# Kernel tuning notes

Hardware: AMD Instinct MI355X
Metric: run time of the kernel (lower is better)

Reference implementation:

```python
import jax, jax.numpy as jnp
import numpy as np

N = 500_000          # n_nodes
E = 16_000_000       # n_edges (avg degree 32)
F0 = 3               # INIT_DIM, input feature dim
H = 32               # hidden units
N_MID = 6            # num_layers=8 -> 1 first + 6 mid + 1 last
ALPHA = 0.9          # self.ALHPA in the original


def setup_inputs() -> dict:
    key = jax.random.key(0)
    ks = jax.random.split(key, 10)
    s = 0.1  # glorot-ish scale for tiny dims
    x = jax.random.normal(ks[0], (N, F0), jnp.float32)
    rows = jax.random.randint(ks[1], (E,), 0, N, jnp.int32)
    cols = jax.random.randint(ks[2], (E,), 0, N, jnp.int32)
    # normalized adjacency values (positive, small, like D^-1/2 A D^-1/2)
    vals = jax.random.uniform(ks[3], (E,), jnp.float32) * 0.1
    w_init0 = jax.random.normal(ks[4], (F0, F0), jnp.float32) * s
    w_x0 = jax.random.normal(ks[5], (F0, H), jnp.float32) * s
    w_init_mid = jax.random.normal(ks[6], (N_MID, F0, H), jnp.float32) * s
    w_x_mid = jax.random.normal(ks[7], (N_MID, H, H), jnp.float32) * s
    w_init_last = jax.random.normal(ks[8], (F0, H), jnp.float32) * s
    w_x_last = jax.random.normal(ks[9], (H, 1), jnp.float32) * s
    return dict(x=x, rows=rows, cols=cols, vals=vals,
                w_init0=w_init0, w_x0=w_x0,
                w_init_mid=w_init_mid, w_x_mid=w_x_mid,
                w_init_last=w_init_last, w_x_last=w_x_last)


def _spmm(rows, cols, vals, x):
    # sparse [N,N] @ dense [N,F] via COO gather + segment scatter-add
    return jax.ops.segment_sum(vals[:, None] * x[cols], rows, num_segments=N)


def _layer(h, x0, rows, cols, vals, w_init, w_x, act):
    agg = _spmm(rows, cols, vals, h)                       # [N, F]
    blend = ALPHA * agg + (1.0 - ALPHA) * (x0 @ w_init)    # alpha-blended residual
    return act(blend @ w_x)                                # dense transform + activation


def reference(x, rows, cols, vals, w_init0, w_x0, w_init_mid, w_x_mid,
              w_init_last, w_x_last):
    x0 = x
    h = _layer(x, x0, rows, cols, vals, w_init0, w_x0, jax.nn.relu)
    for i in range(N_MID):  # fixed small loop over structurally distinct layers
        h = _layer(h, x0, rows, cols, vals, w_init_mid[i], w_x_mid[i], jax.nn.relu)
    return _layer(h, x0, rows, cols, vals, w_init_last, w_x_last, jax.nn.sigmoid)
```

## Files before the change

### kernel.cpp

```cpp
#include <hip/hip_runtime.h>
#include <hip/hip_fp16.h>

#define NN 500000
#define NE 16000000
#define HD 32
#define NMID 6
#define F0 3

#define RPB 1024
#define NBUK ((NN + RPB - 1) / RPB)
#define GRID_P 2048
#define EBLK ((NE + GRID_P - 1) / GRID_P)
#define CAP 21504

static constexpr float ALPHA = 0.9f;
static constexpr float OMA = 1.0f - 0.9f;
static constexpr float VENC = 8191.0f / 0.1f;
static constexpr float VDEC = 0.1f / 8191.0f;

static __device__ __forceinline__ float pk_val(unsigned int w) {
    return (float)(w >> 19) * VDEC;
}

__global__ void prep_pack(const float* __restrict__ w_init_mid,
                          const float* __restrict__ w_x_mid,
                          const float* __restrict__ w_init_last,
                          const float* __restrict__ w_x_last,
                          float4* __restrict__ wpk,
                          float2* __restrict__ wc2,
                          float* __restrict__ wcl) {
    int t = blockIdx.x * 512 + threadIdx.x;
    if (t < 5 * 256) {
        int i = t >> 8, r = t & 255, k = r >> 4, f = r & 15;
        const float* W = w_x_mid + (size_t)(i + 1) * HD * HD;
        wpk[t] = make_float4(W[(2 * k) * HD + 2 * f], W[(2 * k) * HD + 2 * f + 1],
                             W[(2 * k + 1) * HD + 2 * f], W[(2 * k + 1) * HD + 2 * f + 1]);
    } else if (t < 5 * 256 + NMID * 48) {
        int r = t - 1280;
        int i = r / 48, rr = r % 48, k = rr >> 4, f = rr & 15;
        const float* wi = w_init_mid + (size_t)i * F0 * HD;
        const float* wx = w_x_mid + (size_t)i * HD * HD;
        float a = 0.f, b = 0.f;
        for (int j = 0; j < HD; ++j) {
            a += wi[k * HD + j] * wx[j * HD + 2 * f];
            b += wi[k * HD + j] * wx[j * HD + 2 * f + 1];
        }
        wc2[r] = make_float2(OMA * a, OMA * b);
    } else if (t < 1280 + NMID * 48 + F0) {
        int k = t - (1280 + NMID * 48);
        float a = 0.f;
        for (int j = 0; j < HD; ++j) a += w_init_last[k * HD + j] * w_x_last[j];
        wcl[k] = OMA * a;
    }
}

__global__ void prep_xh(const float* __restrict__ x, uint2* __restrict__ xh) {
    int n = blockIdx.x * 256 + threadIdx.x;
    if (n >= NN) return;
    __half2 lo = __floats2half2_rn(x[n * 3 + 0], x[n * 3 + 1]);
    __half2 hi = __floats2half2_rn(x[n * 3 + 2], 0.f);
    xh[n] = make_uint2(*reinterpret_cast<unsigned int*>(&lo),
                       *reinterpret_cast<unsigned int*>(&hi));
}

__global__ void bucket_hist(const int* __restrict__ rows, int* __restrict__ cnt) {
    __shared__ int lh[512];
    int tid = threadIdx.x;
    lh[tid] = 0;
    __syncthreads();
    int e0 = blockIdx.x * EBLK;
    int e1 = min(e0 + EBLK, NE);
    for (int e = e0 + tid; e < e1; e += 512)
        atomicAdd(&lh[rows[e] >> 10], 1);
    __syncthreads();
    if (tid < NBUK && lh[tid]) atomicAdd(&cnt[tid], lh[tid]);
}

__global__ void scan_buckets(int* __restrict__ cnt) {
    __shared__ int s[512];
    int tid = threadIdx.x;
    int v = (tid < NBUK) ? cnt[tid] : 0;
    s[tid] = v;
    __syncthreads();
    for (int off = 1; off < 512; off <<= 1) {
        int t = (tid >= off) ? s[tid - off] : 0;
        __syncthreads();
        s[tid] += t;
        __syncthreads();
    }
    if (tid < NBUK) cnt[tid] = s[tid] - v;
}

__global__ void p1_scatter(const int* __restrict__ rows, const int* __restrict__ cols,
                           const float* __restrict__ vals, int* __restrict__ tail,
                           int2* __restrict__ tmp) {
    __shared__ int lh[512], gb[512], lp[512];
    int tid = threadIdx.x;
    lh[tid] = 0;
    __syncthreads();
    int e0 = blockIdx.x * EBLK;
    int e1 = min(e0 + EBLK, NE);
    for (int e = e0 + tid; e < e1; e += 512)
        atomicAdd(&lh[rows[e] >> 10], 1);
    __syncthreads();
    if (tid < NBUK && lh[tid]) gb[tid] = atomicAdd(&tail[tid], lh[tid]);
    lp[tid] = 0;
    __syncthreads();
    for (int e = e0 + tid; e < e1; e += 512) {
        int r = rows[e];
        int b = r >> 10;
        int loc = atomicAdd(&lp[b], 1);
        int pos = gb[b] + loc;
        tmp[pos] = make_int2(((r & (RPB - 1)) << 19) | cols[e], __float_as_int(vals[e]));
    }
}

__global__ void __launch_bounds__(1024) p2_csr(const int* __restrict__ tail,
                                               const int2* __restrict__ tmp,
                                               int* __restrict__ rp,
                                               unsigned int* __restrict__ espk) {
    __shared__ int a[RPB];
    __shared__ int tl[RPB];
    __shared__ unsigned int lbuf[CAP];
    int b = blockIdx.x, tid = threadIdx.x;
    int estart = (b == 0) ? 0 : tail[b - 1];
    int eend = tail[b];
    a[tid] = 0;
    __syncthreads();
    for (int e = estart + tid; e < eend; e += RPB)
        atomicAdd(&a[(unsigned)tmp[e].x >> 19], 1);
    __syncthreads();
    int myc = a[tid];
    for (int off = 1; off < RPB; off <<= 1) {
        int t = (tid >= off) ? a[tid - off] : 0;
        __syncthreads();
        a[tid] += t;
        __syncthreads();
    }
    int rend = estart + a[tid];
    tl[tid] = rend - myc;
    int grow = b * RPB + tid;
    if (grow < NN) rp[grow] = rend;
    __syncthreads();
    int mid = estart + a[511];
    #pragma unroll
    for (int half = 0; half < 2; ++half) {
        int hstart = (half == 0) ? estart : mid;
        int hend   = (half == 0) ? mid : eend;
        int cnt = hend - hstart;
        if (cnt <= CAP) {
            for (int e = estart + tid; e < eend; e += RPB) {
                int2 t = tmp[e];
                int rl = (unsigned)t.x >> 19;
                if ((rl >> 9) == half) {
                    int pos = atomicAdd(&tl[rl], 1);
                    unsigned int q = __float2uint_rn(__int_as_float(t.y) * VENC);
                    lbuf[pos - hstart] = (q << 19) | ((unsigned)t.x & 0x7FFFFu);
                }
            }
            __syncthreads();
            for (int i = tid; i < cnt; i += RPB)
                espk[hstart + i] = lbuf[i];
            __syncthreads();
        } else {
            for (int e = estart + tid; e < eend; e += RPB) {
                int2 t = tmp[e];
                int rl = (unsigned)t.x >> 19;
                if ((rl >> 9) == half) {
                    int pos = atomicAdd(&tl[rl], 1);
                    unsigned int q = __float2uint_rn(__int_as_float(t.y) * VENC);
                    espk[pos] = (q << 19) | ((unsigned)t.x & 0x7FFFFu);
                }
            }
            __syncthreads();
        }
    }
}

__global__ void layer1_fused(const int* __restrict__ rp, const unsigned int* __restrict__ espk,
                             const uint2* __restrict__ xh,
                             const float* __restrict__ x0, const float* __restrict__ w_init0,
                             const float* __restrict__ w_x0, const float* __restrict__ w_x1,
                             unsigned int* __restrict__ gh_out) {
    int tid = blockIdx.x * 256 + threadIdx.x;
    int n = tid >> 5, f = tid & 31;
    if (n >= NN) return;
    int s = (n == 0) ? 0 : rp[n - 1];
    int e_end = rp[n];
    float a0 = 0.f, a1 = 0.f, a2 = 0.f;
    for (int e = s + f; e < e_end; e += 32) {
        unsigned int w = espk[e];
        int c = w & 0x7FFFF;
        float v = pk_val(w);
        uint2 xw = xh[c];
        __half2 lo = *reinterpret_cast<__half2*>(&xw.x);
        __half2 hi = *reinterpret_cast<__half2*>(&xw.y);
        float2 flo = __half22float2(lo);
        float2 fhi = __half22float2(hi);
        a0 = fmaf(v, flo.x, a0);
        a1 = fmaf(v, flo.y, a1);
        a2 = fmaf(v, fhi.x, a2);
    }
    #pragma unroll
    for (int m = 16; m >= 1; m >>= 1) {
        a0 += __shfl_xor(a0, m, 32);
        a1 += __shfl_xor(a1, m, 32);
        a2 += __shfl_xor(a2, m, 32);
    }
    float p0 = x0[n * 3 + 0], p1 = x0[n * 3 + 1], p2 = x0[n * 3 + 2];
    float b0 = ALPHA * a0 + OMA * (p0 * w_init0[0] + p1 * w_init0[3] + p2 * w_init0[6]);
    float b1 = ALPHA * a1 + OMA * (p0 * w_init0[1] + p1 * w_init0[4] + p2 * w_init0[7]);
    float b2 = ALPHA * a2 + OMA * (p0 * w_init0[2] + p1 * w_init0[5] + p2 * w_init0[8]);
    float h = fmaxf(b0 * w_x0[f] + b1 * w_x0[HD + f] + b2 * w_x0[2 * HD + f], 0.f);
    float o = 0.f;
    #pragma unroll
    for (int k = 0; k < HD; ++k) o += __shfl(h, k, 32) * w_x1[k * HD + f];
    o *= ALPHA;
    float o_hi = __shfl_down(o, 1, 32);
    if ((f & 1) == 0) {
        __half2 hp;
        hp.x = __float2half_rn(o);
        hp.y = __float2half_rn(o_hi);
        gh_out[(size_t)n * 16 + (f >> 1)] = *reinterpret_cast<unsigned int*>(&hp);
    }
}

template<int MODE>
__global__ void mid_fused(const int* __restrict__ rp, const unsigned int* __restrict__ espk,
                          const unsigned int* __restrict__ gh_in,
                          const float* __restrict__ x0,
                          const float2* __restrict__ wc2,
                          const float4* __restrict__ wpk,
                          const float* __restrict__ w_last,
                          float* __restrict__ g1_out,
                          unsigned int* __restrict__ gh_out) {
    int tid = blockIdx.x * 256 + threadIdx.x;
    int n = tid >> 4, f = tid & 15;
    if (n >= NN) return;
    int grp = threadIdx.x >> 4;
    __shared__ unsigned int stage[16][16];
    int s = (n == 0) ? 0 : rp[n - 1];
    int e_end = rp[n];
    float acc0 = 0.f, acc1 = 0.f;
    for (int base = s; base < e_end; base += 16) {
        int e = base + f;
        stage[grp][f] = (e < e_end) ? espk[e] : 0u;
        unsigned int ww[16];
        #pragma unroll
        for (int k = 0; k < 16; ++k) ww[k] = stage[grp][k];
        unsigned int gw[16];
        #pragma unroll
        for (int k = 0; k < 16; ++k) gw[k] = gh_in[((size_t)(ww[k] & 0x7FFFFu) << 4) + f];
        #pragma unroll
        for (int k = 0; k < 16; ++k) {
            float v = pk_val(ww[k]);
            __half2 h2 = *reinterpret_cast<__half2*>(&gw[k]);
            float2 gf = __half22float2(h2);
            acc0 = fmaf(v, gf.x, acc0);
            acc1 = fmaf(v, gf.y, acc1);
        }
    }
    float xa = x0[n * 3 + 0], xb = x0[n * 3 + 1], xc = x0[n * 3 + 2];
    float2 w0 = wc2[f], w1 = wc2[16 + f], w2 = wc2[32 + f];
    float h0 = fmaxf(xa * w0.x + xb * w1.x + xc * w2.x + acc0, 0.f);
    float h1 = fmaxf(xa * w0.y + xb * w1.y + xc * w2.y + acc1, 0.f);
    if (MODE == 0) {
        float o0 = 0.f, o1 = 0.f;
        #pragma unroll
        for (int k = 0; k < 16; ++k) {
            float ha = __shfl(h0, k, 16);
            float hb = __shfl(h1, k, 16);
            float4 w = wpk[k * 16 + f];
            o0 += ha * w.x + hb * w.z;
            o1 += ha * w.y + hb * w.w;
        }
        __half2 hp;
        hp.x = __float2half_rn(ALPHA * o0);
        hp.y = __float2half_rn(ALPHA * o1);
        gh_out[(size_t)n * 16 + f] = *reinterpret_cast<unsigned int*>(&hp);
    } else {
        float2 wl = ((const float2*)w_last)[f];
        float t = h0 * wl.x + h1 * wl.y;
        #pragma unroll
        for (int m = 8; m >= 1; m >>= 1) t += __shfl_xor(t, m, 16);
        if (f == 0) g1_out[n] = ALPHA * t;
    }
}

__global__ void last_fused(const int* __restrict__ rp, const unsigned int* __restrict__ espk,
                           const float* __restrict__ g1, const float* __restrict__ x0,
                           const float* __restrict__ wcL, float* __restrict__ out) {
    int tid = blockIdx.x * 256 + threadIdx.x;
    int n = tid >> 5, f = tid & 31;
    if (n >= NN) return;
    int s = (n == 0) ? 0 : rp[n - 1];
    int e_end = rp[n];
    float acc = 0.f;
    for (int e = s + f; e < e_end; e += 32) {
        unsigned int w = espk[e];
        acc = fmaf(pk_val(w), g1[w & 0x7FFFFu], acc);
    }
    #pragma unroll
    for (int m = 16; m >= 1; m >>= 1) acc += __shfl_xor(acc, m, 32);
    if (f == 0) {
        float z = x0[n * 3 + 0] * wcL[0] + x0[n * 3 + 1] * wcL[1] + x0[n * 3 + 2] * wcL[2] + acc;
        out[n] = 1.f / (1.f + __expf(-z));
    }
}

__global__ void fb_spmm_f3(const int* __restrict__ rows, const int* __restrict__ cols,
                           const float* __restrict__ vals, const float* __restrict__ x,
                           float* __restrict__ agg3) {
    int e = blockIdx.x * blockDim.x + threadIdx.x;
    if (e >= NE) return;
    int r = rows[e], c = cols[e];
    float v = vals[e];
    atomicAdd(&agg3[r * 3 + 0], v * x[c * 3 + 0]);
    atomicAdd(&agg3[r * 3 + 1], v * x[c * 3 + 1]);
    atomicAdd(&agg3[r * 3 + 2], v * x[c * 3 + 2]);
}
__global__ void fb_epilogue1(const float* __restrict__ agg3, const float* __restrict__ x0,
                             const float* __restrict__ w_init0, const float* __restrict__ w_x0,
                             const float* __restrict__ w_x_next, float* __restrict__ g_out) {
    int tid = blockIdx.x * blockDim.x + threadIdx.x;
    int n = tid >> 5, f = tid & 31;
    if (n >= NN) return;
    float a0 = agg3[n * 3 + 0], a1 = agg3[n * 3 + 1], a2 = agg3[n * 3 + 2];
    float p0 = x0[n * 3 + 0], p1 = x0[n * 3 + 1], p2 = x0[n * 3 + 2];
    float b0 = ALPHA * a0 + OMA * (p0 * w_init0[0] + p1 * w_init0[3] + p2 * w_init0[6]);
    float b1 = ALPHA * a1 + OMA * (p0 * w_init0[1] + p1 * w_init0[4] + p2 * w_init0[7]);
    float b2 = ALPHA * a2 + OMA * (p0 * w_init0[2] + p1 * w_init0[5] + p2 * w_init0[8]);
    float h = fmaxf(b0 * w_x0[f] + b1 * w_x0[HD + f] + b2 * w_x0[2 * HD + f], 0.f);
    float acc = 0.f;
    #pragma unroll
    for (int k = 0; k < HD; ++k) acc += __shfl(h, k, 32) * w_x_next[k * HD + f];
    g_out[n * HD + f] = ALPHA * acc;
}
__global__ void fb_seed_mid(const float* __restrict__ x0, const float* __restrict__ wc,
                            float* __restrict__ agg) {
    int tid = blockIdx.x * blockDim.x + threadIdx.x;
    int n = tid >> 5, f = tid & 31;
    if (n >= NN) return;
    agg[n * HD + f] = x0[n * 3 + 0] * wc[f] + x0[n * 3 + 1] * wc[HD + f] + x0[n * 3 + 2] * wc[2 * HD + f];
}
__global__ void fb_spmm_f32(const int* __restrict__ rows, const int* __restrict__ cols,
                            const float* __restrict__ vals, const float* __restrict__ g,
                            float* __restrict__ agg) {
    int tid = blockIdx.x * blockDim.x + threadIdx.x;
    int e = tid >> 5, f = tid & 31;
    if (e >= NE) return;
    atomicAdd(&agg[rows[e] * HD + f], vals[e] * g[cols[e] * HD + f]);
}
__global__ void fb_epilogue_mid(const float* __restrict__ agg, const float* __restrict__ w_x_next,
                                float* __restrict__ g_out) {
    int tid = blockIdx.x * blockDim.x + threadIdx.x;
    int n = tid >> 5, f = tid & 31;
    if (n >= NN) return;
    float h = fmaxf(agg[n * HD + f], 0.f);
    float acc = 0.f;
    #pragma unroll
    for (int k = 0; k < HD; ++k) acc += __shfl(h, k, 32) * w_x_next[k * HD + f];
    g_out[n * HD + f] = ALPHA * acc;
}
__global__ void fb_epilogue_to1(const float* __restrict__ agg, const float* __restrict__ w_x_last,
                                float* __restrict__ g1) {
    int tid = blockIdx.x * blockDim.x + threadIdx.x;
    int n = tid >> 5, f = tid & 31;
    if (n >= NN) return;
    float v = fmaxf(agg[n * HD + f], 0.f) * w_x_last[f];
    #pragma unroll
    for (int m = 16; m >= 1; m >>= 1) v += __shfl_xor(v, m, 32);
    if (f == 0) g1[n] = ALPHA * v;
}
__global__ void fb_seed_last(const float* __restrict__ x0, const float* __restrict__ wcL,
                             float* __restrict__ aggL) {
    int n = blockIdx.x * blockDim.x + threadIdx.x;
    if (n >= NN) return;
    aggL[n] = x0[n * 3 + 0] * wcL[0] + x0[n * 3 + 1] * wcL[1] + x0[n * 3 + 2] * wcL[2];
}
__global__ void fb_spmm_f1(const int* __restrict__ rows, const int* __restrict__ cols,
                           const float* __restrict__ vals, const float* __restrict__ g1,
                           float* __restrict__ aggL) {
    int e = blockIdx.x * blockDim.x + threadIdx.x;
    if (e >= NE) return;
    atomicAdd(&aggL[rows[e]], vals[e] * g1[cols[e]]);
}
__global__ void fb_final_sigmoid(const float* __restrict__ aggL, float* __restrict__ out) {
    int n = blockIdx.x * blockDim.x + threadIdx.x;
    if (n >= NN) return;
    out[n] = 1.f / (1.f + __expf(-aggL[n]));
}
__global__ void fb_prep_weights(const float* __restrict__ w_init_mid,
                                const float* __restrict__ w_x_mid,
                                const float* __restrict__ w_init_last,
                                const float* __restrict__ w_x_last,
                                float* __restrict__ wc_mid,
                                float* __restrict__ wc_last) {
    int t = threadIdx.x;
    if (t < NMID * F0 * HD) {
        int i = t / (F0 * HD);
        int r = t - i * (F0 * HD);
        int k = r / HD, f = r % HD;
        const float* wi = w_init_mid + (size_t)i * F0 * HD;
        const float* wx = w_x_mid + (size_t)i * HD * HD;
        float acc = 0.f;
        for (int j = 0; j < HD; ++j) acc += wi[k * HD + j] * wx[j * HD + f];
        wc_mid[t] = OMA * acc;
    } else if (t < NMID * F0 * HD + F0) {
        int k = t - NMID * F0 * HD;
        float acc = 0.f;
        for (int j = 0; j < HD; ++j) acc += w_init_last[k * HD + j] * w_x_last[j];
        wc_last[k] = OMA * acc;
    }
}

extern "C" void kernel_launch(void* const* d_in, const int* in_sizes, int n_in,
                              void* d_out, int out_size, void* d_ws, size_t ws_size,
                              hipStream_t stream) {
    const float* x           = (const float*)d_in[0];
    const int*   rows        = (const int*)d_in[1];
    const int*   cols        = (const int*)d_in[2];
    const float* vals        = (const float*)d_in[3];
    const float* w_init0     = (const float*)d_in[4];
    const float* w_x0        = (const float*)d_in[5];
    const float* w_init_mid  = (const float*)d_in[6];
    const float* w_x_mid     = (const float*)d_in[7];
    const float* w_init_last = (const float*)d_in[8];
    const float* w_x_last    = (const float*)d_in[9];
    float* out = (float*)d_out;

    const int B = 256;
    const int gridE   = NE / B;
    const int gridN32 = (NN * 32 + B - 1) / B;
    const int gridN16 = (NN * 16 + B - 1) / B;
    const int gridN   = (NN + B - 1) / B;

    const size_t SZ_ES = (size_t)NE * 8;
    const size_t SZ_G  = (size_t)NN * HD * 4;
    const size_t SZ_RP = (size_t)NN * 4;
    const size_t NEED  = SZ_ES + 2 * SZ_G + SZ_RP + 4096 + 4096;

    if (ws_size >= NEED) {
        char* base = (char*)d_ws;
        unsigned int* espk = (unsigned int*)base;
        char* reg2 = base + SZ_ES;
        int2* tmp = (int2*)reg2;
        unsigned int* gA = (unsigned int*)reg2;
        unsigned int* gB = (unsigned int*)(reg2 + (size_t)NN * HD * 2);
        float* g1  = (float*)(reg2 + (size_t)2 * NN * HD * 2);
        uint2* xh  = (uint2*)(reg2 + (size_t)2 * NN * HD * 2 + (size_t)NN * 4);
        float4* wpk = (float4*)(reg2 + 70000000);
        float2* wc2 = (float2*)(reg2 + 70000000 + 5 * 256 * 16);
        float*  wcl = (float*)(reg2 + 70000000 + 5 * 256 * 16 + NMID * 48 * 8);
        int* rp  = (int*)(base + SZ_ES + 2 * SZ_G);
        int* bkt = (int*)(base + SZ_ES + 2 * SZ_G + SZ_RP);

        hipMemsetAsync(bkt, 0, NBUK * sizeof(int), stream);
        bucket_hist<<<GRID_P, 512, 0, stream>>>(rows, bkt);
        scan_buckets<<<1, 512, 0, stream>>>(bkt);
        p1_scatter<<<GRID_P, 512, 0, stream>>>(rows, cols, vals, bkt, tmp);
        p2_csr<<<NBUK, RPB, 0, stream>>>(bkt, tmp, rp, espk);

        prep_pack<<<4, 512, 0, stream>>>(w_init_mid, w_x_mid, w_init_last, w_x_last,
                                         wpk, wc2, wcl);
        prep_xh<<<gridN, B, 0, stream>>>(x, xh);

        layer1_fused<<<gridN32, B, 0, stream>>>(rp, espk, xh, x,
                                                w_init0, w_x0, w_x_mid, gA);
        unsigned int* gin = gA; unsigned int* gout = gB;
        for (int i = 0; i < NMID - 1; ++i) {
            mid_fused<0><<<gridN16, B, 0, stream>>>(rp, espk, gin, x, wc2 + i * 48,
                                                    wpk + i * 256, nullptr, nullptr, gout);
            unsigned int* t = gin; gin = gout; gout = t;
        }
        mid_fused<1><<<gridN16, B, 0, stream>>>(rp, espk, gin, x, wc2 + 5 * 48,
                                                nullptr, w_x_last, g1, nullptr);
        last_fused<<<gridN32, B, 0, stream>>>(rp, espk, g1, x, wcl, out);
    } else {
        char* ws = (char*)d_ws;
        float* g      = (float*)ws;
        float* agg    = (float*)(ws + SZ_G);
        float* wc_mid = (float*)(ws + 2 * SZ_G);
        float* wc_last = wc_mid + NMID * F0 * HD;

        fb_prep_weights<<<1, 1024, 0, stream>>>(w_init_mid, w_x_mid, w_init_last, w_x_last,
                                                wc_mid, wc_last);
        hipMemsetAsync(agg, 0, (size_t)NN * 3 * sizeof(float), stream);
        fb_spmm_f3<<<gridE, B, 0, stream>>>(rows, cols, vals, x, agg);
        fb_epilogue1<<<gridN32, B, 0, stream>>>(agg, x, w_init0, w_x0, w_x_mid, g);
        const int gridE32 = (int)(((size_t)NE * 32) / B);
        for (int i = 0; i < NMID; ++i) {
            fb_seed_mid<<<gridN32, B, 0, stream>>>(x, wc_mid + i * F0 * HD, agg);
            fb_spmm_f32<<<gridE32, B, 0, stream>>>(rows, cols, vals, g, agg);
            if (i < NMID - 1)
                fb_epilogue_mid<<<gridN32, B, 0, stream>>>(agg, w_x_mid + (size_t)(i + 1) * HD * HD, g);
            else
                fb_epilogue_to1<<<gridN32, B, 0, stream>>>(agg, w_x_last, g);
        }
        fb_seed_last<<<gridN, B, 0, stream>>>(x, wc_last, agg);
        fb_spmm_f1<<<gridE, B, 0, stream>>>(rows, cols, vals, g, agg);
        fb_final_sigmoid<<<gridN, B, 0, stream>>>(agg, out);
    }
}
```

Before: 2.297 ms.

## Replace global histogram and scatter with block-local sort plus offset directory

The separate bucket-histogram pass and the scatter pass with global atomics are merged into one kernel, p1_sort. Each block sorts its edge chunk by bucket in LDS staging and writes it out contiguously, along with a per-block table of bucket offsets. A small reduction kernel sums that table into bucket counts, and the CSR build kernel then walks each block's segment for its bucket through the table. This removes one full read of rows, the memset and the global atomics, and makes the tmp writes coalesced. In exchange, the CSR kernel reads short per-thread segments serially, which is less coalesced, and p1_sort uses a large LDS staging buffer that may lower occupancy.

After: 2.351 ms. 1.02x slower.

```diff
diff --git a/kernel.cpp b/kernel.cpp
--- a/kernel.cpp
+++ b/kernel.cpp
@@ -12,6 +12,7 @@
 #define GRID_P 2048
 #define EBLK ((NE + GRID_P - 1) / GRID_P)
 #define CAP 21504
+#define DSTR (NBUK + 1)
 
 static constexpr float ALPHA = 0.9f;
 static constexpr float OMA = 1.0f - 0.9f;
@@ -63,17 +64,59 @@
                        *reinterpret_cast<unsigned int*>(&hi));
 }
 
-__global__ void bucket_hist(const int* __restrict__ rows, int* __restrict__ cnt) {
+__global__ void __launch_bounds__(512) p1_sort(const int* __restrict__ rows,
+                                               const int* __restrict__ cols,
+                                               const float* __restrict__ vals,
+                                               int2* __restrict__ tmp,
+                                               int* __restrict__ dir) {
     __shared__ int lh[512];
-    int tid = threadIdx.x;
+    __shared__ int lp[512];
+    __shared__ int2 stg[EBLK];
+    int tid = threadIdx.x, blk = blockIdx.x;
+    int e0 = blk * EBLK, e1 = min(e0 + EBLK, NE);
     lh[tid] = 0;
     __syncthreads();
-    int e0 = blockIdx.x * EBLK;
-    int e1 = min(e0 + EBLK, NE);
     for (int e = e0 + tid; e < e1; e += 512)
         atomicAdd(&lh[rows[e] >> 10], 1);
     __syncthreads();
-    if (tid < NBUK && lh[tid]) atomicAdd(&cnt[tid], lh[tid]);
+    int v = lh[tid];
+    for (int off = 1; off < 512; off <<= 1) {
+        int t = (tid >= off) ? lh[tid - off] : 0;
+        __syncthreads();
+        lh[tid] += t;
+        __syncthreads();
+    }
+    lp[tid] = lh[tid] - v;
+    if (tid < NBUK) dir[(size_t)blk * DSTR + tid] = lp[tid];
+    if (tid == 0)   dir[(size_t)blk * DSTR + NBUK] = e1 - e0;
+    __syncthreads();
+    for (int e = e0 + tid; e < e1; e += 512) {
+        int r = rows[e];
+        int b = r >> 10;
+        int pos = atomicAdd(&lp[b], 1);
+        stg[pos] = make_int2(((r & (RPB - 1)) << 19) | cols[e], __float_as_int(vals[e]));
+    }
+    __syncthreads();
+    int cnt = e1 - e0;
+    for (int i = tid; i < cnt; i += 512)
+        tmp[(size_t)e0 + i] = stg[i];
+}
+
+__global__ void sum_dir(const int* __restrict__ dir, int* __restrict__ cnt) {
+    __shared__ int s[256];
+    int b = blockIdx.x, tid = threadIdx.x;
+    int acc = 0;
+    for (int rblk = tid; rblk < GRID_P; rblk += 256) {
+        const int* d = dir + (size_t)rblk * DSTR + b;
+        acc += d[1] - d[0];
+    }
+    s[tid] = acc;
+    __syncthreads();
+    for (int off = 128; off > 0; off >>= 1) {
+        if (tid < off) s[tid] += s[tid + off];
+        __syncthreads();
+    }
+    if (tid == 0) cnt[b] = s[0];
 }
 
 __global__ void scan_buckets(int* __restrict__ cnt) {
@@ -91,44 +134,24 @@
     if (tid < NBUK) cnt[tid] = s[tid] - v;
 }
 
-__global__ void p1_scatter(const int* __restrict__ rows, const int* __restrict__ cols,
-                           const float* __restrict__ vals, int* __restrict__ tail,
-                           int2* __restrict__ tmp) {
-    __shared__ int lh[512], gb[512], lp[512];
-    int tid = threadIdx.x;
-    lh[tid] = 0;
-    __syncthreads();
-    int e0 = blockIdx.x * EBLK;
-    int e1 = min(e0 + EBLK, NE);
-    for (int e = e0 + tid; e < e1; e += 512)
-        atomicAdd(&lh[rows[e] >> 10], 1);
-    __syncthreads();
-    if (tid < NBUK && lh[tid]) gb[tid] = atomicAdd(&tail[tid], lh[tid]);
-    lp[tid] = 0;
-    __syncthreads();
-    for (int e = e0 + tid; e < e1; e += 512) {
-        int r = rows[e];
-        int b = r >> 10;
-        int loc = atomicAdd(&lp[b], 1);
-        int pos = gb[b] + loc;
-        tmp[pos] = make_int2(((r & (RPB - 1)) << 19) | cols[e], __float_as_int(vals[e]));
-    }
-}
-
-__global__ void __launch_bounds__(1024) p2_csr(const int* __restrict__ tail,
+__global__ void __launch_bounds__(1024) p2_csr(const int* __restrict__ dir,
                                                const int2* __restrict__ tmp,
+                                               const int* __restrict__ bkt,
                                                int* __restrict__ rp,
                                                unsigned int* __restrict__ espk) {
     __shared__ int a[RPB];
     __shared__ int tl[RPB];
     __shared__ unsigned int lbuf[CAP];
     int b = blockIdx.x, tid = threadIdx.x;
-    int estart = (b == 0) ? 0 : tail[b - 1];
-    int eend = tail[b];
     a[tid] = 0;
     __syncthreads();
-    for (int e = estart + tid; e < eend; e += RPB)
-        atomicAdd(&a[(unsigned)tmp[e].x >> 19], 1);
+    for (int rblk = tid; rblk < GRID_P; rblk += RPB) {
+        const int* d = dir + (size_t)rblk * DSTR + b;
+        int lo = d[0], hi = d[1];
+        const int2* base = tmp + (size_t)rblk * EBLK;
+        for (int i = lo; i < hi; ++i)
+            atomicAdd(&a[(unsigned)base[i].x >> 19], 1);
+    }
     __syncthreads();
     int myc = a[tid];
     for (int off = 1; off < RPB; off <<= 1) {
@@ -137,25 +160,32 @@
         a[tid] += t;
         __syncthreads();
     }
+    int estart = bkt[b];
     int rend = estart + a[tid];
     tl[tid] = rend - myc;
     int grow = b * RPB + tid;
     if (grow < NN) rp[grow] = rend;
     __syncthreads();
-    int mid = estart + a[511];
+    int mid  = estart + a[511];
+    int eend = estart + a[RPB - 1];
     #pragma unroll
     for (int half = 0; half < 2; ++half) {
         int hstart = (half == 0) ? estart : mid;
         int hend   = (half == 0) ? mid : eend;
         int cnt = hend - hstart;
         if (cnt <= CAP) {
-            for (int e = estart + tid; e < eend; e += RPB) {
-                int2 t = tmp[e];
-                int rl = (unsigned)t.x >> 19;
-                if ((rl >> 9) == half) {
-                    int pos = atomicAdd(&tl[rl], 1);
-                    unsigned int q = __float2uint_rn(__int_as_float(t.y) * VENC);
-                    lbuf[pos - hstart] = (q << 19) | ((unsigned)t.x & 0x7FFFFu);
+            for (int rblk = tid; rblk < GRID_P; rblk += RPB) {
+                const int* d = dir + (size_t)rblk * DSTR + b;
+                int lo = d[0], hi = d[1];
+                const int2* base = tmp + (size_t)rblk * EBLK;
+                for (int i = lo; i < hi; ++i) {
+                    int2 t = base[i];
+                    int rl = (unsigned)t.x >> 19;
+                    if ((rl >> 9) == half) {
+                        int pos = atomicAdd(&tl[rl], 1);
+                        unsigned int q = __float2uint_rn(__int_as_float(t.y) * VENC);
+                        lbuf[pos - hstart] = (q << 19) | ((unsigned)t.x & 0x7FFFFu);
+                    }
                 }
             }
             __syncthreads();
@@ -163,13 +193,18 @@
                 espk[hstart + i] = lbuf[i];
             __syncthreads();
         } else {
-            for (int e = estart + tid; e < eend; e += RPB) {
-                int2 t = tmp[e];
-                int rl = (unsigned)t.x >> 19;
-                if ((rl >> 9) == half) {
-                    int pos = atomicAdd(&tl[rl], 1);
-                    unsigned int q = __float2uint_rn(__int_as_float(t.y) * VENC);
-                    espk[pos] = (q << 19) | ((unsigned)t.x & 0x7FFFFu);
+            for (int rblk = tid; rblk < GRID_P; rblk += RPB) {
+                const int* d = dir + (size_t)rblk * DSTR + b;
+                int lo = d[0], hi = d[1];
+                const int2* base = tmp + (size_t)rblk * EBLK;
+                for (int i = lo; i < hi; ++i) {
+                    int2 t = base[i];
+                    int rl = (unsigned)t.x >> 19;
+                    if ((rl >> 9) == half) {
+                        int pos = atomicAdd(&tl[rl], 1);
+                        unsigned int q = __float2uint_rn(__int_as_float(t.y) * VENC);
+                        espk[pos] = (q << 19) | ((unsigned)t.x & 0x7FFFFu);
+                    }
                 }
             }
             __syncthreads();
@@ -443,6 +478,7 @@
     if (ws_size >= NEED) {
         char* base = (char*)d_ws;
         unsigned int* espk = (unsigned int*)base;
+        int* dir = (int*)(base + (size_t)NE * 4);
         char* reg2 = base + SZ_ES;
         int2* tmp = (int2*)reg2;
         unsigned int* gA = (unsigned int*)reg2;
@@ -455,11 +491,10 @@
         int* rp  = (int*)(base + SZ_ES + 2 * SZ_G);
         int* bkt = (int*)(base + SZ_ES + 2 * SZ_G + SZ_RP);
 
-        hipMemsetAsync(bkt, 0, NBUK * sizeof(int), stream);
-        bucket_hist<<<GRID_P, 512, 0, stream>>>(rows, bkt);
+        p1_sort<<<GRID_P, 512, 0, stream>>>(rows, cols, vals, tmp, dir);
+        sum_dir<<<NBUK, 256, 0, stream>>>(dir, bkt);
         scan_buckets<<<1, 512, 0, stream>>>(bkt);
-        p1_scatter<<<GRID_P, 512, 0, stream>>>(rows, cols, vals, bkt, tmp);
-        p2_csr<<<NBUK, RPB, 0, stream>>>(bkt, tmp, rp, espk);
+        p2_csr<<<NBUK, RPB, 0, stream>>>(dir, tmp, bkt, rp, espk);
 
         prep_pack<<<4, 512, 0, stream>>>(w_init_mid, w_x_mid, w_init_last, w_x_last,
                                          wpk, wc2, wcl);
```
